# Performance work log

Measured on AMD Instinct MI355X. Metric: run time of the kernel, lower is better.

Reference implementation:

```python
import jax, jax.numpy as jnp
import numpy as np

K_BINS = 2048
EMB = 64
MU = 0.99
THRESHOLD = 1.0


def setup_inputs() -> dict:
    key = jax.random.key(0)
    kx, kk = jax.random.split(key)
    x = jax.random.normal(kx, (131072, EMB), dtype=jnp.float32)
    k = jax.random.normal(kk, (K_BINS, EMB), dtype=jnp.float32)
    # restore_k semantics: k_sum starts as a copy of k, k_elem as ones
    return {"x": x, "k": k, "k_sum": k, "k_elem": jnp.ones((K_BINS,), jnp.float32)}


def reference(x, k, k_sum, k_elem):
    N, T = x.shape  # T == EMB (preprocess branch 1)
    # preprocess: prenorm statistic
    prenorm = jnp.linalg.norm(x - jnp.mean(x)) / np.sqrt(x.size)

    # quantise: squared-L2 distance to codebook, argmin, fit
    dist = (jnp.sum(x * x, axis=-1, keepdims=True)
            - 2.0 * (x @ k.T)
            + jnp.sum(k * k, axis=-1)[None, :])  # (N, K_BINS)
    x_l = jnp.argmin(dist, axis=-1)               # (N,)
    fit = jnp.mean(jnp.min(dist, axis=-1))

    # dequantise: codebook gather
    x_d = k[x_l]                                  # (N, EMB)

    # update_k (torch.no_grad block): EMA codebook update
    _k_sum = jax.ops.segment_sum(x, x_l, num_segments=K_BINS)          # == onehot @ x
    _k_elem = jax.ops.segment_sum(jnp.ones((N,), x.dtype), x_l, num_segments=K_BINS)
    # N >= K_BINS so _tile is identity; randperm -> deterministic jax perm
    perm = jax.random.permutation(jax.random.key(42), N)
    _k_rand = x[perm[:K_BINS]]                    # (K_BINS, EMB)
    new_k_sum = MU * k_sum + (1.0 - MU) * _k_sum
    new_k_elem = MU * k_elem + (1.0 - MU) * _k_elem
    usage = (new_k_elem[:, None] >= THRESHOLD).astype(x.dtype)
    new_k = usage * (new_k_sum / new_k_elem[:, None]) + (1.0 - usage) * _k_rand
    _k_prob = _k_elem / jnp.sum(_k_elem)
    entropy = -jnp.sum(_k_prob * jnp.log(_k_prob + 1e-8))
    used_curr = jnp.sum((_k_elem >= THRESHOLD).astype(jnp.int32))
    usage_total = jnp.sum(usage)
    dk = jnp.linalg.norm(new_k - k) / np.sqrt(new_k.size)

    # commit loss (x_d detached) and straight-through estimator
    commit_loss = jnp.sum((jax.lax.stop_gradient(x_d) - x) ** 2) / x.size
    x_d_st = x + jax.lax.stop_gradient(x_d - x)

    # postprocess: view(N, T, -1).permute(0, 2, 1) -> (N, 1, EMB)
    x_d_out = x_d_st.reshape(N, T, -1).transpose(0, 2, 1)
    return (x_l, x_d_out, commit_loss, fit, prenorm,
            entropy, used_curr, usage_total, dk,
            new_k, new_k_sum, new_k_elem)
```

## Files before the change

### kernel.cpp

```cpp
#include <hip/hip_runtime.h>
#include <stdint.h>

#define N_ROWS 131072
#define DIM 64
#define KB 2048
#define M_ELEMS 8388608

#define O_XL   0
#define O_XD   131072
#define O_CL   8519680
#define O_FIT  8519681
#define O_PRE  8519682
#define O_ENT  8519683
#define O_USED 8519684
#define O_UTOT 8519685
#define O_DK   8519686
#define O_NK   8519687
#define O_NKS  8650759
#define O_NKE  8781831

#define A_DBL   0
#define A_CNT   64
#define A_KK2N  128
#define A_KST   8320
#define A_XLI   532608
#define A_KCNT  1056896
#define A_BCUR  1065088
#define A_KRAND 1073280
#define A_BOFF  1597568
#define A_FLAG  1605760
#define A_ROWL  2130048
#define A_KS64  2654336
#define A_BITS  1605760
#define A_PKEY  2130048
#define A_HIST  3702912
#define A_BSUM  3833984
#define A_CUR   3834496
#define A_PIDX  3965568
#define A_RES1  4489856
#define WS_END  5014144

typedef short bf16x8 __attribute__((ext_vector_type(8)));
typedef float f32x4 __attribute__((ext_vector_type(4)));

#define GLL16(G, L) __builtin_amdgcn_global_load_lds( \
    (const __attribute__((address_space(1))) void*)(G), \
    (__attribute__((address_space(3))) void*)(L), 16, 0, 0)
#define GLL4(G, L) __builtin_amdgcn_global_load_lds( \
    (const __attribute__((address_space(1))) void*)(G), \
    (__attribute__((address_space(3))) void*)(L), 4, 0, 0)


__device__ __forceinline__ float block_reduce_sum(float v, float* lds) {
  #pragma unroll
  for (int off = 32; off > 0; off >>= 1) v += __shfl_down(v, off, 64);
  int lane = threadIdx.x & 63, wid = threadIdx.x >> 6;
  if (lane == 0) lds[wid] = v;
  __syncthreads();
  float r = 0.f;
  if (threadIdx.x == 0) {
    int nw = blockDim.x >> 6;
    for (int i = 0; i < nw; ++i) r += lds[i];
  }
  __syncthreads();
  return r;
}

__device__ __forceinline__ unsigned short f2bf_rne(float f) {
  uint32_t u = __float_as_uint(f);
  uint32_t r = u + 0x7FFFu + ((u >> 16) & 1u);
  return (unsigned short)(r >> 16);
}

#define TF_ROUND(r) do { x0 += x1; x1 = (x1 << (r)) | (x1 >> (32 - (r))); x1 ^= x0; } while (0)

__device__ __forceinline__ void threefry2x32(uint32_t k0, uint32_t k1,
                                             uint32_t c0, uint32_t c1,
                                             uint32_t& o0, uint32_t& o1) {
  uint32_t k2 = k0 ^ k1 ^ 0x1BD11BDAu;
  uint32_t x0 = c0 + k0, x1 = c1 + k1;
  TF_ROUND(13); TF_ROUND(15); TF_ROUND(26); TF_ROUND(6);
  x0 += k1; x1 += k2 + 1u;
  TF_ROUND(17); TF_ROUND(29); TF_ROUND(16); TF_ROUND(24);
  x0 += k2; x1 += k0 + 2u;
  TF_ROUND(13); TF_ROUND(15); TF_ROUND(26); TF_ROUND(6);
  x0 += k0; x1 += k1 + 3u;
  TF_ROUND(17); TF_ROUND(29); TF_ROUND(16); TF_ROUND(24);
  x0 += k1; x1 += k2 + 4u;
  TF_ROUND(13); TF_ROUND(15); TF_ROUND(26); TF_ROUND(6);
  x0 += k2; x1 += k0 + 5u;
  o0 = x0; o1 = x1;
}

__global__ __launch_bounds__(256) void k_prep(
    const float* __restrict__ k, unsigned short* __restrict__ kst,
    float* __restrict__ kk2n) {
  int w = (blockIdx.x * blockDim.x + threadIdx.x) >> 6;
  int lane = threadIdx.x & 63;
  float v = k[(size_t)w * DIM + lane];
  unsigned short h = f2bf_rne(v);
  float hf = __uint_as_float((uint32_t)h << 16);
  unsigned short lo = f2bf_rne(v - hf);
  int t = w >> 4, r = w & 15;
  int c = lane >> 3, e = lane & 7;
  int slot = c ^ (r & 7);
  size_t u16i = (size_t)t * 2048 + r * 64 + slot * 8 + e;
  kst[u16i] = h;
  kst[u16i + 1024] = lo;
  float q = v * v;
  #pragma unroll
  for (int off = 32; off > 0; off >>= 1) q += __shfl_down(q, off, 64);
  if (lane == 0) kk2n[w] = -0.5f * q;
}

__global__ __launch_bounds__(256) void k_main(
    const float* __restrict__ x, const float* __restrict__ korig,
    const unsigned short* __restrict__ kst, const float* __restrict__ kk2n,
    int* __restrict__ xli, uint32_t* __restrict__ flag, int* __restrict__ cnt,
    float* __restrict__ out, double* __restrict__ dbl) {
  __shared__ __align__(16) char smem[2][16640];
  __shared__ float lds_red[4];
  int tid = threadIdx.x;
  int lane = tid & 63;
  int wid = tid >> 6;
  int lrow = lane & 15;
  int lk = lane >> 4;
  int r0 = (blockIdx.x * 4 + wid) * 32;

  bf16x8 xh[2][2], xl[2][2];
  float qrow[2] = {0.f, 0.f};
  float s_acc = 0.f;
  #pragma unroll
  for (int g = 0; g < 2; ++g) {
    #pragma unroll
    for (int kt = 0; kt < 2; ++kt) {
      const float* xp = x + (size_t)(r0 + g * 16 + lrow) * DIM + kt * 32 + lk * 8;
      float4 v0 = *(const float4*)xp;
      float4 v1 = *(const float4*)(xp + 4);
      float vv[8] = {v0.x, v0.y, v0.z, v0.w, v1.x, v1.y, v1.z, v1.w};
      #pragma unroll
      for (int i = 0; i < 8; ++i) {
        float v = vv[i];
        s_acc += v;
        qrow[g] = fmaf(v, v, qrow[g]);
        unsigned short h = f2bf_rne(v);
        float hf = __uint_as_float((uint32_t)h << 16);
        xh[g][kt][i] = (short)h;
        xl[g][kt][i] = (short)f2bf_rne(v - hf);
      }
    }
  }
  float bs = block_reduce_sum(s_acc, lds_red);
  float bq = block_reduce_sum(qrow[0] + qrow[1], lds_red);
  if (tid == 0) {
    atomicAdd(&dbl[0], (double)bs);
    atomicAdd(&dbl[1], (double)bq);
  }

  int offH0 = lrow * 128 + (((lk    ) ^ (lrow & 7)) << 4);
  int offH1 = lrow * 128 + (((lk + 4) ^ (lrow & 7)) << 4);

  const char* kst_b = (const char*)kst;
  const char* kk_b  = (const char*)kk2n;

  {
    char* ldst = &smem[0][0];
    #pragma unroll
    for (int c = 0; c < 4; ++c)
      GLL16(kst_b + c * 4096 + tid * 16, ldst + c * 4096 + tid * 16);
    if (wid == 0) GLL4(kk_b + lane * 4, ldst + 16384 + lane * 4);
  }

  float b1[2], b2[2];
  uint32_t j1[2];
  #pragma unroll
  for (int g = 0; g < 2; ++g) {
    b1[g] = -3.402823466e38f; b2[g] = -3.402823466e38f; j1[g] = 0;
  }

  for (int t = 0; t < 32; ++t) {
    __syncthreads();
    if (t + 1 < 32) {
      const char* gsrc = kst_b + (size_t)(t + 1) * 16384;
      char* ldst = &smem[(t + 1) & 1][0];
      #pragma unroll
      for (int c = 0; c < 4; ++c)
        GLL16(gsrc + c * 4096 + tid * 16, ldst + c * 4096 + tid * 16);
      if (wid == 0) GLL4(kk_b + (size_t)(t + 1) * 256 + lane * 4, ldst + 16384 + lane * 4);
    }
    const char* B = &smem[t & 1][0];
    #pragma unroll
    for (int s = 0; s < 4; ++s) {
      bf16x8 ah0 = *(const bf16x8*)(B + s * 4096 + offH0);
      bf16x8 ah1 = *(const bf16x8*)(B + s * 4096 + offH1);
      bf16x8 al0 = *(const bf16x8*)(B + s * 4096 + 2048 + offH0);
      bf16x8 al1 = *(const bf16x8*)(B + s * 4096 + 2048 + offH1);
      f32x4 kkv  = *(const f32x4*)(B + 16384 + s * 64 + lk * 16);
      uint32_t jb = (uint32_t)(t * 64 + s * 16 + lk * 4);
      #pragma unroll
      for (int g = 0; g < 2; ++g) {
        f32x4 acc = __builtin_amdgcn_mfma_f32_16x16x32_bf16(ah0, xh[g][0], kkv, 0, 0, 0);
        acc = __builtin_amdgcn_mfma_f32_16x16x32_bf16(ah1, xh[g][1], acc, 0, 0, 0);
        acc = __builtin_amdgcn_mfma_f32_16x16x32_bf16(al0, xh[g][0], acc, 0, 0, 0);
        acc = __builtin_amdgcn_mfma_f32_16x16x32_bf16(al1, xh[g][1], acc, 0, 0, 0);
        acc = __builtin_amdgcn_mfma_f32_16x16x32_bf16(ah0, xl[g][0], acc, 0, 0, 0);
        acc = __builtin_amdgcn_mfma_f32_16x16x32_bf16(ah1, xl[g][1], acc, 0, 0, 0);
        #pragma unroll
        for (int reg = 0; reg < 4; ++reg) {
          float v = acc[reg];
          bool gt = v > b1[g];
          float mn = fminf(v, b1[g]);
          b2[g] = fmaxf(b2[g], mn);
          b1[g] = gt ? v : b1[g];
          j1[g] = gt ? (jb + (uint32_t)reg) : j1[g];
        }
      }
    }
  }

  float cl_acc = 0.f;
  #pragma unroll
  for (int g = 0; g < 2; ++g) {
    float xxr = qrow[g];
    #pragma unroll
    for (int s = 16; s <= 32; s <<= 1) {
      float ob1 = __shfl_xor(b1[g], s, 64);
      float ob2 = __shfl_xor(b2[g], s, 64);
      uint32_t oj1 = __shfl_xor(j1[g], s, 64);
      xxr += __shfl_xor(xxr, s, 64);
      bool gt = ob1 > b1[g];
      float mn = fminf(b1[g], ob1);
      b2[g] = fmaxf(fmaxf(b2[g], ob2), mn);
      b1[g] = fmaxf(b1[g], ob1);
      j1[g] = gt ? oj1 : j1[g];
    }
    int row = r0 + g * 16 + lrow;
    {
      const float4* kp = (const float4*)(korig + (size_t)j1[g] * DIM + lk * 16);
      float4* xd = (float4*)(out + O_XD + (size_t)row * DIM + lk * 16);
      #pragma unroll
      for (int q = 0; q < 4; ++q) xd[q] = kp[q];
    }
    if (lk == 0) {
      xli[row] = (int)j1[g];
      out[O_XL + row] = (float)j1[g];
      cl_acc += fmaf(-2.f, b1[g], xxr);
      if (b1[g] - b2[g] < 0.01f) {
        int i = atomicAdd(cnt, 1);
        flag[i] = (uint32_t)row;
      }
    }
  }
  float bc = block_reduce_sum(cl_acc, lds_red);
  if (tid == 0) atomicAdd(&dbl[2], (double)bc);
}

__global__ __launch_bounds__(256) void k_rescan(
    const uint32_t* __restrict__ flag, const int* __restrict__ cnt,
    const float* __restrict__ x, const float* __restrict__ k,
    int* __restrict__ xli, float* __restrict__ out, double* __restrict__ dbl) {
  __shared__ float xs[4][64];
  int lane = threadIdx.x & 63;
  int wid = threadIdx.x >> 6;
  int gw = (blockIdx.x * blockDim.x + threadIdx.x) >> 6;
  int n = *cnt;
  for (int fi = gw; fi < n; fi += 1024) {
    int row = flag[fi];
    int jold = xli[row];
    xs[wid][lane] = x[(size_t)row * DIM + lane];
    double bd = 1e300;
    double eold = 0.0;
    int bj = 0;
    for (int j = lane; j < KB; j += 64) {
      const float* kr = k + (size_t)j * DIM;
      double e = 0.0;
      #pragma unroll
      for (int d = 0; d < DIM; ++d) {
        double diff = (double)xs[wid][d] - (double)kr[d];
        e = fma(diff, diff, e);
      }
      if (e < bd) { bd = e; bj = j; }
      if (j == jold) eold = e;
    }
    #pragma unroll
    for (int off = 32; off > 0; off >>= 1) {
      double od = __shfl_down(bd, off, 64);
      int oj = __shfl_down(bj, off, 64);
      eold += __shfl_down(eold, off, 64);
      if (od < bd || (od == bd && oj < bj)) { bd = od; bj = oj; }
    }
    int bjf = __shfl(bj, 0, 64);
    if (bjf != jold) {
      out[O_XD + (size_t)row * DIM + lane] = k[(size_t)bjf * DIM + lane];
      if (lane == 0) {
        xli[row] = bjf;
        out[O_XL + row] = (float)bjf;
        atomicAdd(&dbl[2], bd - eold);
      }
    }
  }
}

__global__ void k_hist_rows(const int* __restrict__ xli, int* __restrict__ kcnt) {
  int i = blockIdx.x * blockDim.x + threadIdx.x;
  atomicAdd(&kcnt[xli[i]], 1);
}


__global__ __launch_bounds__(1024) void k_scan_bins(const int* __restrict__ kcnt,
                                                    uint32_t* __restrict__ boffs) {
  __shared__ uint32_t part[1024];
  int tid = threadIdx.x;
  uint32_t c0 = (uint32_t)kcnt[2 * tid];
  uint32_t c1 = (uint32_t)kcnt[2 * tid + 1];
  part[tid] = c0 + c1;
  __syncthreads();
  for (int off = 1; off < 1024; off <<= 1) {
    uint32_t v = (tid >= off) ? part[tid - off] : 0u;
    __syncthreads();
    part[tid] += v;
    __syncthreads();
  }
  uint32_t run = (tid > 0) ? part[tid - 1] : 0u;
  boffs[2 * tid] = run;
  boffs[2 * tid + 1] = run + c0;
}

__global__ void k_scatter_rows(const int* __restrict__ xli, const uint32_t* __restrict__ boffs,
                               uint32_t* __restrict__ bcur, uint32_t* __restrict__ rowlist) {
  int i = blockIdx.x * blockDim.x + threadIdx.x;
  int b = xli[i];
  uint32_t pos = boffs[b] + atomicAdd(&bcur[b], 1u);
  rowlist[pos] = (uint32_t)i;
}

__global__ __launch_bounds__(256) void k_segsum(
    const uint32_t* __restrict__ rowlist, const int* __restrict__ xli,
    const float* __restrict__ x, double* __restrict__ ks64) {
  int gw = (blockIdx.x * blockDim.x + threadIdx.x) >> 6;
  int lane = threadIdx.x & 63;
  uint32_t p0 = (uint32_t)gw * 16;
  double acc = 0.0;
  int cur = -1;
  #pragma unroll 4
  for (int i = 0; i < 16; ++i) {
    uint32_t row = rowlist[p0 + i];
    int bin = xli[row];
    if (bin != cur) {
      if (cur >= 0) atomicAdd(&ks64[(size_t)cur * DIM + lane], acc);
      acc = 0.0; cur = bin;
    }
    acc += (double)x[(size_t)row * DIM + lane];
  }
  if (cur >= 0) atomicAdd(&ks64[(size_t)cur * DIM + lane], acc);
}


__global__ void k_bits_hist(int which, uint32_t* __restrict__ bits,
                            uint32_t* __restrict__ hist) {
  uint32_t a0, a1, b0, b1;
  threefry2x32(0u, 42u, 0u, 2u, a0, b0);
  threefry2x32(0u, 42u, 1u, 3u, a1, b1);
  uint32_t k0, k1;
  if (which == 0) { k0 = b0; k1 = b1; }
  else {
    uint32_t c0, c1, d0, d1;
    threefry2x32(a0, a1, 0u, 2u, c0, d0);
    threefry2x32(a0, a1, 1u, 3u, c1, d1);
    k0 = d0; k1 = d1;
  }
  int i = blockIdx.x * blockDim.x + threadIdx.x;
  uint32_t y0, y1;
  threefry2x32(k0, k1, (uint32_t)i, (uint32_t)(i + 65536), y0, y1);
  bits[i] = y0;
  bits[i + 65536] = y1;
  atomicAdd(&hist[y0 >> 17], 1u);
  atomicAdd(&hist[y1 >> 17], 1u);
}

__global__ __launch_bounds__(256) void k_scanA(uint32_t* __restrict__ hist,
                                               uint32_t* __restrict__ bsum) {
  __shared__ uint32_t sh[256];
  int tid = threadIdx.x;
  int bin = blockIdx.x * 256 + tid;
  uint32_t v = hist[bin];
  sh[tid] = v;
  __syncthreads();
  for (int off = 1; off < 256; off <<= 1) {
    uint32_t t = (tid >= off) ? sh[tid - off] : 0u;
    __syncthreads();
    sh[tid] += t;
    __syncthreads();
  }
  hist[bin] = sh[tid] - v;
  if (tid == 255) bsum[blockIdx.x] = sh[tid];
}

__global__ void k_scanB(uint32_t* __restrict__ bsum) {
  __shared__ uint32_t sh[128];
  int tid = threadIdx.x;
  uint32_t v = bsum[tid];
  sh[tid] = v;
  __syncthreads();
  for (int off = 1; off < 128; off <<= 1) {
    uint32_t t = (tid >= off) ? sh[tid - off] : 0u;
    __syncthreads();
    sh[tid] += t;
    __syncthreads();
  }
  bsum[tid] = sh[tid] - v;
}

__global__ void k_scatter(const uint32_t* __restrict__ bits, const uint32_t* __restrict__ hist,
                          const uint32_t* __restrict__ bsum, uint32_t* __restrict__ cursor,
                          uint32_t* __restrict__ pkey, uint32_t* __restrict__ pidx) {
  int i = blockIdx.x * blockDim.x + threadIdx.x;
  uint32_t key = bits[i];
  uint32_t bin = key >> 17;
  uint32_t pos = hist[bin] + bsum[bin >> 8] + atomicAdd(&cursor[bin], 1u);
  pkey[pos] = key; pidx[pos] = (uint32_t)i;
}

__global__ void k_rank(const uint32_t* __restrict__ pkey, const uint32_t* __restrict__ pidx,
                       const uint32_t* __restrict__ hist, const uint32_t* __restrict__ bsum,
                       const uint32_t* __restrict__ cursor,
                       const uint32_t* __restrict__ srcvals, uint32_t* __restrict__ outv,
                       const float* __restrict__ x, float* __restrict__ krand,
                       int limit) {
  int s = blockIdx.x * blockDim.x + threadIdx.x;
  uint32_t myk = pkey[s], myi = pidx[s];
  uint32_t bin = myk >> 17;
  uint32_t start = hist[bin] + bsum[bin >> 8], cntb = cursor[bin];
  uint32_t r = 0;
  for (uint32_t t = 0; t < cntb; ++t) {
    uint32_t ok = pkey[start + t], oi = pidx[start + t];
    r += (ok < myk || (ok == myk && oi < myi)) ? 1u : 0u;
  }
  uint32_t pos = start + r;
  if (limit == 0) {
    outv[pos] = myi;
  } else if (pos < (uint32_t)limit) {
    uint32_t orig = srcvals[myi];
    const float4* xs = (const float4*)(x + (size_t)orig * DIM);
    float4* kd = (float4*)(krand + (size_t)pos * DIM);
    #pragma unroll
    for (int q = 0; q < 16; ++q) kd[q] = xs[q];
  }
}


__global__ __launch_bounds__(256) void k_elem_kernel(
    const double* __restrict__ ks64, const int* __restrict__ kcnt,
    const float* __restrict__ k_sum_in, const float* __restrict__ k_elem_in,
    const float* __restrict__ k_in, const float* __restrict__ krand,
    float* __restrict__ out, double* __restrict__ dbl) {
  __shared__ float lds[8];
  const float OMF = (float)(1.0 - 0.99);
  int e = blockIdx.x * blockDim.x + threadIdx.x;
  int b = e >> 6;
  float part = (float)ks64[e];
  float nks = 0.99f * k_sum_in[e] + OMF * part;
  out[O_NKS + e] = nks;
  float cnt = (float)kcnt[b];
  float ke = 0.99f * k_elem_in[b] + OMF * cnt;
  float nk = (ke >= 1.f) ? (nks / ke) : krand[e];
  out[O_NK + e] = nk;
  float dd = nk - k_in[e];
  float bsum = block_reduce_sum(dd * dd, lds);
  if (threadIdx.x == 0) atomicAdd(&dbl[4], (double)bsum);
}

__global__ __launch_bounds__(1024) void k_finale(
    const int* __restrict__ kcnt, const float* __restrict__ k_elem_in,
    float* __restrict__ out, const double* __restrict__ dbl) {
  __shared__ float ent_l[1024];
  __shared__ int u1_l[1024], u2_l[1024];
  const float OMF = (float)(1.0 - 0.99);
  int tid = threadIdx.x;
  float ent = 0.f; int used = 0, usage = 0;
  #pragma unroll
  for (int t = 0; t < 2; ++t) {
    int b = tid + t * 1024;
    float cnt = (float)kcnt[b];
    float ke = 0.99f * k_elem_in[b] + OMF * cnt;
    out[O_NKE + b] = ke;
    float p = cnt * (1.f / 131072.f);
    ent -= p * logf(p + 1e-8f);
    used += (cnt >= 1.f) ? 1 : 0;
    usage += (ke >= 1.f) ? 1 : 0;
  }
  ent_l[tid] = ent; u1_l[tid] = used; u2_l[tid] = usage;
  __syncthreads();
  for (int off = 512; off > 0; off >>= 1) {
    if (tid < off) {
      ent_l[tid] += ent_l[tid + off];
      u1_l[tid] += u1_l[tid + off];
      u2_l[tid] += u2_l[tid + off];
    }
    __syncthreads();
  }
  if (tid == 0) {
    double M = (double)M_ELEMS;
    double sumS = dbl[0], sumQ = dbl[1];
    double var = (sumQ - sumS * sumS / M) / M;
    out[O_PRE] = (float)sqrt(var > 0.0 ? var : 0.0);
    out[O_FIT] = (float)(dbl[2] / (double)N_ROWS);
    out[O_CL]  = (float)(dbl[2] / M);
    out[O_DK]  = (float)sqrt(dbl[4] / (double)(KB * DIM));
    out[O_ENT] = ent_l[0];
    out[O_USED] = (float)u1_l[0];
    out[O_UTOT] = (float)u2_l[0];
  }
}


extern "C" void kernel_launch(void* const* d_in, const int* in_sizes, int n_in,
                              void* d_out, int out_size, void* d_ws, size_t ws_size,
                              hipStream_t stream) {
  (void)in_sizes; (void)n_in; (void)out_size; (void)ws_size;
  const float* x      = (const float*)d_in[0];
  const float* k      = (const float*)d_in[1];
  const float* k_sum  = (const float*)d_in[2];
  const float* k_elem = (const float*)d_in[3];
  float* out = (float*)d_out;
  char* ws = (char*)d_ws;

  double*   dbl   = (double*)(ws + A_DBL);
  int*      cnt   = (int*)(ws + A_CNT);
  float*    kk2n  = (float*)(ws + A_KK2N);
  unsigned short* kst = (unsigned short*)(ws + A_KST);
  int*      xli   = (int*)(ws + A_XLI);
  int*      kcnt  = (int*)(ws + A_KCNT);
  uint32_t* bcur  = (uint32_t*)(ws + A_BCUR);
  float*    krand = (float*)(ws + A_KRAND);
  uint32_t* boffs = (uint32_t*)(ws + A_BOFF);
  uint32_t* flag  = (uint32_t*)(ws + A_FLAG);
  uint32_t* rowl  = (uint32_t*)(ws + A_ROWL);
  double*   ks64  = (double*)(ws + A_KS64);
  uint32_t* bits  = (uint32_t*)(ws + A_BITS);
  uint32_t* pkey  = (uint32_t*)(ws + A_PKEY);
  uint32_t* hist  = (uint32_t*)(ws + A_HIST);
  uint32_t* bsum  = (uint32_t*)(ws + A_BSUM);
  uint32_t* cur   = (uint32_t*)(ws + A_CUR);
  uint32_t* pidx  = (uint32_t*)(ws + A_PIDX);
  uint32_t* res1  = (uint32_t*)(ws + A_RES1);

  (void)hipMemsetAsync(ws + A_DBL, 0, 128, stream);
  (void)hipMemsetAsync(ws + A_KCNT, 0, 16384, stream);
  (void)hipMemsetAsync(ws + A_KS64, 0, 1048576, stream);

  k_prep<<<512, 256, 0, stream>>>(k, kst, kk2n);
  k_main<<<1024, 256, 0, stream>>>(x, k, kst, kk2n, xli, flag, cnt, out, dbl);
  k_rescan<<<256, 256, 0, stream>>>(flag, cnt, x, k, xli, out, dbl);

  k_hist_rows<<<512, 256, 0, stream>>>(xli, kcnt);
  k_scan_bins<<<1, 1024, 0, stream>>>(kcnt, boffs);
  k_scatter_rows<<<512, 256, 0, stream>>>(xli, boffs, bcur, rowl);
  k_segsum<<<2048, 256, 0, stream>>>(rowl, xli, x, ks64);

  (void)hipMemsetAsync(ws + A_HIST, 0, 262656, stream);
  k_bits_hist<<<256, 256, 0, stream>>>(0, bits, hist);
  k_scanA<<<128, 256, 0, stream>>>(hist, bsum);
  k_scanB<<<1, 128, 0, stream>>>(bsum);
  k_scatter<<<512, 256, 0, stream>>>(bits, hist, bsum, cur, pkey, pidx);
  k_rank<<<512, 256, 0, stream>>>(pkey, pidx, hist, bsum, cur, nullptr, res1,
                                  nullptr, nullptr, 0);
  (void)hipMemsetAsync(ws + A_HIST, 0, 262656, stream);
  k_bits_hist<<<256, 256, 0, stream>>>(1, bits, hist);
  k_scanA<<<128, 256, 0, stream>>>(hist, bsum);
  k_scanB<<<1, 128, 0, stream>>>(bsum);
  k_scatter<<<512, 256, 0, stream>>>(bits, hist, bsum, cur, pkey, pidx);
  k_rank<<<512, 256, 0, stream>>>(pkey, pidx, hist, bsum, cur, res1, nullptr,
                                  x, krand, 2048);

  k_elem_kernel<<<512, 256, 0, stream>>>(ks64, kcnt, k_sum, k_elem, k, krand, out, dbl);
  k_finale<<<1, 1024, 0, stream>>>(kcnt, k_elem, out, dbl);
}
```

Measured before the change: 374.6 us.

## Double rows per wave in distance kernel, fold bsum scan, merge memsets

```diff
diff --git a/kernel.cpp b/kernel.cpp
--- a/kernel.cpp
+++ b/kernel.cpp
@@ -21,18 +21,18 @@
 
 #define A_DBL   0
 #define A_CNT   64
-#define A_KK2N  128
-#define A_KST   8320
-#define A_XLI   532608
-#define A_KCNT  1056896
-#define A_BCUR  1065088
-#define A_KRAND 1073280
-#define A_BOFF  1597568
-#define A_FLAG  1605760
-#define A_ROWL  2130048
-#define A_KS64  2654336
-#define A_BITS  1605760
-#define A_PKEY  2130048
+#define A_KCNT  128
+#define A_BCUR  8320
+#define A_KS64  16512
+#define A_KK2N  1065088
+#define A_KST   1073280
+#define A_XLI   1597568
+#define A_KRAND 2121856
+#define A_BOFF  2646144
+#define A_FLAG  2654336
+#define A_ROWL  3178624
+#define A_BITS  2654336
+#define A_PKEY  3178624
 #define A_HIST  3702912
 #define A_BSUM  3833984
 #define A_CUR   3834496
@@ -90,6 +90,19 @@
   TF_ROUND(13); TF_ROUND(15); TF_ROUND(26); TF_ROUND(6);
   x0 += k2; x1 += k0 + 5u;
   o0 = x0; o1 = x1;
+}
+
+__device__ __forceinline__ void local_bsum_scan(const uint32_t* __restrict__ bsum,
+                                                uint32_t* sb) {
+  int tid = threadIdx.x;
+  if (tid < 128) sb[tid] = bsum[tid];
+  __syncthreads();
+  for (int off = 1; off < 128; off <<= 1) {
+    uint32_t t = (tid < 128 && tid >= off) ? sb[tid - off] : 0u;
+    __syncthreads();
+    if (tid < 128) sb[tid] += t;
+    __syncthreads();
+  }
 }
 
 __global__ __launch_bounds__(256) void k_prep(
@@ -125,13 +138,13 @@
   int wid = tid >> 6;
   int lrow = lane & 15;
   int lk = lane >> 4;
-  int r0 = (blockIdx.x * 4 + wid) * 32;
-
-  bf16x8 xh[2][2], xl[2][2];
-  float qrow[2] = {0.f, 0.f};
+  int r0 = (blockIdx.x * 4 + wid) * 64;
+
+  bf16x8 xh[4][2], xl[4][2];
+  float qrow[4] = {0.f, 0.f, 0.f, 0.f};
   float s_acc = 0.f;
   #pragma unroll
-  for (int g = 0; g < 2; ++g) {
+  for (int g = 0; g < 4; ++g) {
     #pragma unroll
     for (int kt = 0; kt < 2; ++kt) {
       const float* xp = x + (size_t)(r0 + g * 16 + lrow) * DIM + kt * 32 + lk * 8;
@@ -151,7 +164,7 @@
     }
   }
   float bs = block_reduce_sum(s_acc, lds_red);
-  float bq = block_reduce_sum(qrow[0] + qrow[1], lds_red);
+  float bq = block_reduce_sum(qrow[0] + qrow[1] + qrow[2] + qrow[3], lds_red);
   if (tid == 0) {
     atomicAdd(&dbl[0], (double)bs);
     atomicAdd(&dbl[1], (double)bq);
@@ -171,10 +184,10 @@
     if (wid == 0) GLL4(kk_b + lane * 4, ldst + 16384 + lane * 4);
   }
 
-  float b1[2], b2[2];
-  uint32_t j1[2];
+  float b1[4], b2[4];
+  uint32_t j1[4];
   #pragma unroll
-  for (int g = 0; g < 2; ++g) {
+  for (int g = 0; g < 4; ++g) {
     b1[g] = -3.402823466e38f; b2[g] = -3.402823466e38f; j1[g] = 0;
   }
 
@@ -189,6 +202,7 @@
       if (wid == 0) GLL4(kk_b + (size_t)(t + 1) * 256 + lane * 4, ldst + 16384 + lane * 4);
     }
     const char* B = &smem[t & 1][0];
+    __builtin_amdgcn_s_setprio(1);
     #pragma unroll
     for (int s = 0; s < 4; ++s) {
       bf16x8 ah0 = *(const bf16x8*)(B + s * 4096 + offH0);
@@ -198,7 +212,7 @@
       f32x4 kkv  = *(const f32x4*)(B + 16384 + s * 64 + lk * 16);
       uint32_t jb = (uint32_t)(t * 64 + s * 16 + lk * 4);
       #pragma unroll
-      for (int g = 0; g < 2; ++g) {
+      for (int g = 0; g < 4; ++g) {
         f32x4 acc = __builtin_amdgcn_mfma_f32_16x16x32_bf16(ah0, xh[g][0], kkv, 0, 0, 0);
         acc = __builtin_amdgcn_mfma_f32_16x16x32_bf16(ah1, xh[g][1], acc, 0, 0, 0);
         acc = __builtin_amdgcn_mfma_f32_16x16x32_bf16(al0, xh[g][0], acc, 0, 0, 0);
@@ -216,11 +230,12 @@
         }
       }
     }
+    __builtin_amdgcn_s_setprio(0);
   }
 
   float cl_acc = 0.f;
   #pragma unroll
-  for (int g = 0; g < 2; ++g) {
+  for (int g = 0; g < 4; ++g) {
     float xxr = qrow[g];
     #pragma unroll
     for (int s = 16; s <= 32; s <<= 1) {
@@ -396,41 +411,37 @@
   if (tid == 255) bsum[blockIdx.x] = sh[tid];
 }
 
-__global__ void k_scanB(uint32_t* __restrict__ bsum) {
-  __shared__ uint32_t sh[128];
-  int tid = threadIdx.x;
-  uint32_t v = bsum[tid];
-  sh[tid] = v;
-  __syncthreads();
-  for (int off = 1; off < 128; off <<= 1) {
-    uint32_t t = (tid >= off) ? sh[tid - off] : 0u;
-    __syncthreads();
-    sh[tid] += t;
-    __syncthreads();
-  }
-  bsum[tid] = sh[tid] - v;
-}
-
-__global__ void k_scatter(const uint32_t* __restrict__ bits, const uint32_t* __restrict__ hist,
-                          const uint32_t* __restrict__ bsum, uint32_t* __restrict__ cursor,
-                          uint32_t* __restrict__ pkey, uint32_t* __restrict__ pidx) {
+__global__ __launch_bounds__(256) void k_scatter(
+    const uint32_t* __restrict__ bits, const uint32_t* __restrict__ hist,
+    const uint32_t* __restrict__ bsum, uint32_t* __restrict__ cursor,
+    uint32_t* __restrict__ pkey, uint32_t* __restrict__ pidx) {
+  __shared__ uint32_t sb[128];
+  local_bsum_scan(bsum, sb);
   int i = blockIdx.x * blockDim.x + threadIdx.x;
   uint32_t key = bits[i];
   uint32_t bin = key >> 17;
-  uint32_t pos = hist[bin] + bsum[bin >> 8] + atomicAdd(&cursor[bin], 1u);
+  uint32_t blk = bin >> 8;
+  uint32_t base = (blk ? sb[blk - 1] : 0u);
+  uint32_t pos = hist[bin] + base + atomicAdd(&cursor[bin], 1u);
   pkey[pos] = key; pidx[pos] = (uint32_t)i;
 }
 
-__global__ void k_rank(const uint32_t* __restrict__ pkey, const uint32_t* __restrict__ pidx,
-                       const uint32_t* __restrict__ hist, const uint32_t* __restrict__ bsum,
-                       const uint32_t* __restrict__ cursor,
-                       const uint32_t* __restrict__ srcvals, uint32_t* __restrict__ outv,
-                       const float* __restrict__ x, float* __restrict__ krand,
-                       int limit) {
+__global__ __launch_bounds__(256) void k_rank(
+    const uint32_t* __restrict__ pkey, const uint32_t* __restrict__ pidx,
+    const uint32_t* __restrict__ hist, const uint32_t* __restrict__ bsum,
+    const uint32_t* __restrict__ cursor,
+    const uint32_t* __restrict__ srcvals, uint32_t* __restrict__ outv,
+    const float* __restrict__ x, float* __restrict__ krand,
+    int limit) {
+  __shared__ uint32_t sb[128];
+  local_bsum_scan(bsum, sb);
   int s = blockIdx.x * blockDim.x + threadIdx.x;
   uint32_t myk = pkey[s], myi = pidx[s];
   uint32_t bin = myk >> 17;
-  uint32_t start = hist[bin] + bsum[bin >> 8], cntb = cursor[bin];
+  uint32_t blk = bin >> 8;
+  uint32_t start = hist[bin] + (blk ? sb[blk - 1] : 0u);
+  uint32_t cntb = cursor[bin];
+  if (limit != 0 && start >= (uint32_t)limit) return;
   uint32_t r = 0;
   for (uint32_t t = 0; t < cntb; ++t) {
     uint32_t ok = pkey[start + t], oi = pidx[start + t];
@@ -527,16 +538,16 @@
 
   double*   dbl   = (double*)(ws + A_DBL);
   int*      cnt   = (int*)(ws + A_CNT);
+  int*      kcnt  = (int*)(ws + A_KCNT);
+  uint32_t* bcur  = (uint32_t*)(ws + A_BCUR);
+  double*   ks64  = (double*)(ws + A_KS64);
   float*    kk2n  = (float*)(ws + A_KK2N);
   unsigned short* kst = (unsigned short*)(ws + A_KST);
   int*      xli   = (int*)(ws + A_XLI);
-  int*      kcnt  = (int*)(ws + A_KCNT);
-  uint32_t* bcur  = (uint32_t*)(ws + A_BCUR);
   float*    krand = (float*)(ws + A_KRAND);
   uint32_t* boffs = (uint32_t*)(ws + A_BOFF);
   uint32_t* flag  = (uint32_t*)(ws + A_FLAG);
   uint32_t* rowl  = (uint32_t*)(ws + A_ROWL);
-  double*   ks64  = (double*)(ws + A_KS64);
   uint32_t* bits  = (uint32_t*)(ws + A_BITS);
   uint32_t* pkey  = (uint32_t*)(ws + A_PKEY);
   uint32_t* hist  = (uint32_t*)(ws + A_HIST);
@@ -545,12 +556,10 @@
   uint32_t* pidx  = (uint32_t*)(ws + A_PIDX);
   uint32_t* res1  = (uint32_t*)(ws + A_RES1);
 
-  (void)hipMemsetAsync(ws + A_DBL, 0, 128, stream);
-  (void)hipMemsetAsync(ws + A_KCNT, 0, 16384, stream);
-  (void)hipMemsetAsync(ws + A_KS64, 0, 1048576, stream);
+  (void)hipMemsetAsync(ws, 0, 1065088, stream);
 
   k_prep<<<512, 256, 0, stream>>>(k, kst, kk2n);
-  k_main<<<1024, 256, 0, stream>>>(x, k, kst, kk2n, xli, flag, cnt, out, dbl);
+  k_main<<<512, 256, 0, stream>>>(x, k, kst, kk2n, xli, flag, cnt, out, dbl);
   k_rescan<<<256, 256, 0, stream>>>(flag, cnt, x, k, xli, out, dbl);
 
   k_hist_rows<<<512, 256, 0, stream>>>(xli, kcnt);
@@ -561,14 +570,12 @@
   (void)hipMemsetAsync(ws + A_HIST, 0, 262656, stream);
   k_bits_hist<<<256, 256, 0, stream>>>(0, bits, hist);
   k_scanA<<<128, 256, 0, stream>>>(hist, bsum);
-  k_scanB<<<1, 128, 0, stream>>>(bsum);
   k_scatter<<<512, 256, 0, stream>>>(bits, hist, bsum, cur, pkey, pidx);
   k_rank<<<512, 256, 0, stream>>>(pkey, pidx, hist, bsum, cur, nullptr, res1,
                                   nullptr, nullptr, 0);
   (void)hipMemsetAsync(ws + A_HIST, 0, 262656, stream);
   k_bits_hist<<<256, 256, 0, stream>>>(1, bits, hist);
   k_scanA<<<128, 256, 0, stream>>>(hist, bsum);
-  k_scanB<<<1, 128, 0, stream>>>(bsum);
   k_scatter<<<512, 256, 0, stream>>>(bits, hist, bsum, cur, pkey, pidx);
   k_rank<<<512, 256, 0, stream>>>(pkey, pidx, hist, bsum, cur, res1, nullptr,
                                   x, krand, 2048);
```

Measured after the change: 359.6 us. 1.04x faster.
